# Kernel tuning notes

Hardware: AMD Instinct MI355X
Metric: run time of the kernel (lower is better)

Reference implementation:

```python
import jax, jax.numpy as jnp
import numpy as np

N, LDIMS, HID, HID2 = 1024, 256, 128, 64


def setup_inputs() -> dict:
    key = jax.random.key(0)
    ks = jax.random.split(key, 8)
    return {
        "x": jax.random.normal(ks[0], (N, 2, LDIMS), dtype=jnp.float32),
        "W_foh": jax.random.normal(ks[1], (2 * LDIMS, HID), dtype=jnp.float32) * 0.05,
        "W_fom": jax.random.normal(ks[2], (2 * LDIMS, HID), dtype=jnp.float32) * 0.05,
        "cat_bias": jax.random.normal(ks[3], (2 * HID,), dtype=jnp.float32) * 0.05,
        "W_hid2": jax.random.normal(ks[4], (2 * HID, HID2), dtype=jnp.float32) * 0.05,
        "hid2_bias": jax.random.normal(ks[5], (HID2,), dtype=jnp.float32) * 0.05,
        "W_out": jax.random.normal(ks[6], (HID2, 1), dtype=jnp.float32) * 0.05,
        "out_bias": jax.random.normal(ks[7], (1,), dtype=jnp.float32) * 0.05,
    }


def reference(x, W_foh, W_fom, cat_bias, W_hid2, hid2_bias, W_out, out_bias):
    n = x.shape[0]
    h = W_foh.shape[1]
    xf = x.reshape(n, -1)                      # concat(lstms_0, lstms_1) -> [n, 2*ldims]
    headfov = xf @ W_foh                       # [n, h]
    modfov = xf @ W_fom                        # [n, h]
    # Original: tanh(concat(headfov_i, modfov_j) + catBias) @ W_hid2.
    # tanh is elementwise, and concat @ W_hid2 splits exactly into top/bottom blocks,
    # so we precompute per-node terms instead of materializing [n, n, 2h].
    th = jnp.tanh(headfov + cat_bias[:h]) @ W_hid2[:h]    # [n, hid2]
    tm = jnp.tanh(modfov + cat_bias[h:]) @ W_hid2[h:]     # [n, hid2]
    pre = th[:, None, :] + tm[None, :, :] + hid2_bias     # [n, n, hid2]
    h2 = jnp.tanh(pre)
    scores = jnp.einsum('ijd,do->ijo', h2, W_out)[..., 0] + out_bias[0]  # [n, n]
    return scores
```

## Files before the change

### kernel.cpp

```cpp
#include <hip/hip_runtime.h>
#include <hip/hip_bf16.h>
#include <stdint.h>

typedef __attribute__((ext_vector_type(8))) short bf16x8;
typedef __attribute__((ext_vector_type(4))) float f32x4;

#define NN 1024
#define KD 512
#define NC 256
#define H2 64

#define OFF_A    0
#define OFF_WT   1048576
#define OFF_WHB  1310720
#define OFF_G    1343488
#define OFF_PT   1867776
#define OFF_QT   2129920

#define TANH_SCALE 2.8853900817779268f

static __device__ __forceinline__ ushort f2bf(float f) {
    uint32_t u = __builtin_bit_cast(uint32_t, f);
    uint32_t r = (u + 0x7fffu + ((u >> 16) & 1u)) >> 16;
    return (ushort)r;
}

__global__ __launch_bounds__(256) void k0_pack(const float* __restrict__ x,
                                               const float* __restrict__ W_foh,
                                               const float* __restrict__ W_fom,
                                               const float* __restrict__ W_hid2,
                                               ushort* __restrict__ A,
                                               ushort* __restrict__ Wt,
                                               ushort* __restrict__ Whb) {
    int tid = blockIdx.x * 256 + threadIdx.x;
    if (tid < 131072) {
        float4 v = ((const float4*)x)[tid];
        ushort4 o;
        o.x = f2bf(v.x); o.y = f2bf(v.y); o.z = f2bf(v.z); o.w = f2bf(v.w);
        ((ushort4*)A)[tid] = o;
    } else if (tid < 262144) {
        int t2 = tid - 131072;
        int c = t2 & 255, k = t2 >> 8;
        float v = (c < 128) ? W_foh[k * 128 + c] : W_fom[k * 128 + c - 128];
        Wt[c * 512 + k] = f2bf(v);
    } else if (tid < 278528) {
        int t3 = tid - 262144;
        int d = t3 & 63, c = t3 >> 6;
        Whb[d * 256 + c] = f2bf(W_hid2[c * 64 + d]);
    }
}

__global__ __launch_bounds__(256) void k1_gemm1(const ushort* __restrict__ A,
                                                const ushort* __restrict__ Wt,
                                                const float* __restrict__ cat_bias,
                                                ushort* __restrict__ g) {
    int lane = threadIdx.x & 63;
    int wave = threadIdx.x >> 6;
    int b = blockIdx.x;
    int ntile = b & 15;
    int mtile = (b >> 4) * 4 + wave;
    int l15 = lane & 15;
    int kofs = (lane >> 4) * 8;
    const ushort* Ar = A + (mtile * 16 + l15) * 512 + kofs;
    const ushort* Br = Wt + (ntile * 16 + l15) * 512 + kofs;
    f32x4 acc = {0.f, 0.f, 0.f, 0.f};
#pragma unroll
    for (int s = 0; s < 16; ++s) {
        bf16x8 a = *(const bf16x8*)(Ar + s * 32);
        bf16x8 bb = *(const bf16x8*)(Br + s * 32);
        acc = __builtin_amdgcn_mfma_f32_16x16x32_bf16(a, bb, acc, 0, 0, 0);
    }
    int col = ntile * 16 + l15;
    float cb = cat_bias[col];
#pragma unroll
    for (int r = 0; r < 4; ++r) {
        int row = mtile * 16 + (lane >> 4) * 4 + r;
        float xv = acc[r] + cb;
        float e = exp2f(xv * TANH_SCALE);
        float t = 1.0f - 2.0f * __builtin_amdgcn_rcpf(e + 1.0f);
        g[row * 256 + col] = f2bf(t);
    }
}

__global__ __launch_bounds__(256) void k2_gemm2(const ushort* __restrict__ g,
                                                const ushort* __restrict__ Whb,
                                                const float* __restrict__ hid2_bias,
                                                float* __restrict__ Pt,
                                                float* __restrict__ Qt) {
    int lane = threadIdx.x & 63;
    int wv = blockIdx.x * 4 + (threadIdx.x >> 6);
    int mtile = wv & 63;
    int dtile = (wv >> 6) & 3;
    int half = wv >> 8;
    int cbase = half * 128;
    int l15 = lane & 15;
    int kofs = (lane >> 4) * 8;
    const ushort* Ar = g + (mtile * 16 + l15) * 256 + cbase + kofs;
    const ushort* Br = Whb + (dtile * 16 + l15) * 256 + cbase + kofs;
    f32x4 acc = {0.f, 0.f, 0.f, 0.f};
#pragma unroll
    for (int s = 0; s < 4; ++s) {
        bf16x8 a = *(const bf16x8*)(Ar + s * 32);
        bf16x8 bb = *(const bf16x8*)(Br + s * 32);
        acc = __builtin_amdgcn_mfma_f32_16x16x32_bf16(a, bb, acc, 0, 0, 0);
    }
    int dcol = dtile * 16 + l15;
    float* out = half ? Qt : Pt;
    float badd = half ? 0.0f : hid2_bias[dcol];
#pragma unroll
    for (int r = 0; r < 4; ++r) {
        int i = mtile * 16 + (lane >> 4) * 4 + r;
        out[dcol * 1024 + i] = (acc[r] + badd) * TANH_SCALE;
    }
}

__global__ __launch_bounds__(256) void k3_scores(const float* __restrict__ Pt,
                                                 const float* __restrict__ Qt,
                                                 const float* __restrict__ W_out,
                                                 const float* __restrict__ out_bias,
                                                 float* __restrict__ out) {
    __shared__ float Pl[64][68];
    __shared__ float Ql[64][68];
    __shared__ float wl[64];
    int t = threadIdx.x;
    int b = blockIdx.x;
    int i0 = (b >> 4) * 64;
    int j0 = (b & 15) * 64;
    {
        int rowd = t >> 2;
        int cch = (t & 3) * 16;
        const float4* ps = (const float4*)(Pt + rowd * 1024 + i0 + cch);
        const float4* qs = (const float4*)(Qt + rowd * 1024 + j0 + cch);
#pragma unroll
        for (int u = 0; u < 4; ++u) {
            *(float4*)(&Pl[rowd][cch + u * 4]) = ps[u];
            *(float4*)(&Ql[rowd][cch + u * 4]) = qs[u];
        }
    }
    if (t < 64) wl[t] = -2.0f * W_out[t];
    float base = out_bias[0];
#pragma unroll
    for (int d = 0; d < 64; ++d) base += W_out[d];
    __syncthreads();

    int il = (t & 15) * 4;
    int jl = (t >> 4) * 4;
    float acc[4][4] = {};
#pragma unroll 4
    for (int d = 0; d < 64; ++d) {
        f32x4 p = *(const f32x4*)(&Pl[d][il]);
        f32x4 q = *(const f32x4*)(&Ql[d][jl]);
        float w = wl[d];
#pragma unroll
        for (int a = 0; a < 4; ++a)
#pragma unroll
            for (int c = 0; c < 4; ++c) {
                float e = exp2f(p[a] + q[c]);
                float r = __builtin_amdgcn_rcpf(e + 1.0f);
                acc[a][c] = fmaf(w, r, acc[a][c]);
            }
    }
#pragma unroll
    for (int a = 0; a < 4; ++a) {
        float4 v;
        v.x = base + acc[a][0];
        v.y = base + acc[a][1];
        v.z = base + acc[a][2];
        v.w = base + acc[a][3];
        *(float4*)(&out[(i0 + il + a) * 1024 + j0 + jl]) = v;
    }
}

extern "C" void kernel_launch(void* const* d_in, const int* in_sizes, int n_in,
                              void* d_out, int out_size, void* d_ws, size_t ws_size,
                              hipStream_t stream) {
    const float* x        = (const float*)d_in[0];
    const float* W_foh    = (const float*)d_in[1];
    const float* W_fom    = (const float*)d_in[2];
    const float* cat_bias = (const float*)d_in[3];
    const float* W_hid2   = (const float*)d_in[4];
    const float* hid2_bias= (const float*)d_in[5];
    const float* W_out    = (const float*)d_in[6];
    const float* out_bias = (const float*)d_in[7];

    char* ws = (char*)d_ws;
    ushort* A   = (ushort*)(ws + OFF_A);
    ushort* Wt  = (ushort*)(ws + OFF_WT);
    ushort* Whb = (ushort*)(ws + OFF_WHB);
    ushort* g   = (ushort*)(ws + OFF_G);
    float*  Pt  = (float*)(ws + OFF_PT);
    float*  Qt  = (float*)(ws + OFF_QT);

    k0_pack<<<1088, 256, 0, stream>>>(x, W_foh, W_fom, W_hid2, A, Wt, Whb);
    k1_gemm1<<<256, 256, 0, stream>>>(A, Wt, cat_bias, g);
    k2_gemm2<<<128, 256, 0, stream>>>(g, Whb, hid2_bias, Pt, Qt);
    k3_scores<<<256, 256, 0, stream>>>(Pt, Qt, W_out, out_bias, (float*)d_out);
}
```

Baseline: 104.4 us.

## Split-K gemm1 across waves and halve score tile width for more blocks

The first GEMM now splits the K dimension across the four waves of a block and reduces the partial sums through shared memory, launching four times as many blocks. The scores kernel uses 64x32 tiles instead of 64x64, doubling the block count to 512 so more CUs are occupied. The aim is to fill the 256-CU device better in both kernels. The cost is an extra shared-memory reduction and barrier in gemm1, and more redundant P loads per output in the scores kernel.

```diff
diff --git a/kernel.cpp b/kernel.cpp
--- a/kernel.cpp
+++ b/kernel.cpp
@@ -54,31 +54,40 @@
                                                 const ushort* __restrict__ Wt,
                                                 const float* __restrict__ cat_bias,
                                                 ushort* __restrict__ g) {
+    __shared__ float red[4 * 64 * 4];
     int lane = threadIdx.x & 63;
     int wave = threadIdx.x >> 6;
     int b = blockIdx.x;
     int ntile = b & 15;
-    int mtile = (b >> 4) * 4 + wave;
+    int mtile = b >> 4;
     int l15 = lane & 15;
-    int kofs = (lane >> 4) * 8;
+    int kofs = wave * 128 + (lane >> 4) * 8;
     const ushort* Ar = A + (mtile * 16 + l15) * 512 + kofs;
     const ushort* Br = Wt + (ntile * 16 + l15) * 512 + kofs;
     f32x4 acc = {0.f, 0.f, 0.f, 0.f};
 #pragma unroll
-    for (int s = 0; s < 16; ++s) {
+    for (int s = 0; s < 4; ++s) {
         bf16x8 a = *(const bf16x8*)(Ar + s * 32);
         bf16x8 bb = *(const bf16x8*)(Br + s * 32);
         acc = __builtin_amdgcn_mfma_f32_16x16x32_bf16(a, bb, acc, 0, 0, 0);
     }
-    int col = ntile * 16 + l15;
-    float cb = cat_bias[col];
-#pragma unroll
-    for (int r = 0; r < 4; ++r) {
-        int row = mtile * 16 + (lane >> 4) * 4 + r;
-        float xv = acc[r] + cb;
-        float e = exp2f(xv * TANH_SCALE);
-        float t = 1.0f - 2.0f * __builtin_amdgcn_rcpf(e + 1.0f);
-        g[row * 256 + col] = f2bf(t);
+    *(f32x4*)(&red[(wave * 64 + lane) * 4]) = acc;
+    __syncthreads();
+    if (wave == 0) {
+        f32x4 s0 = *(const f32x4*)(&red[(0 * 64 + lane) * 4]);
+        f32x4 s1 = *(const f32x4*)(&red[(1 * 64 + lane) * 4]);
+        f32x4 s2 = *(const f32x4*)(&red[(2 * 64 + lane) * 4]);
+        f32x4 s3 = *(const f32x4*)(&red[(3 * 64 + lane) * 4]);
+        int col = ntile * 16 + l15;
+        float cb = cat_bias[col];
+#pragma unroll
+        for (int r = 0; r < 4; ++r) {
+            int row = mtile * 16 + (lane >> 4) * 4 + r;
+            float xv = s0[r] + s1[r] + s2[r] + s3[r] + cb;
+            float e = exp2f(xv * TANH_SCALE);
+            float t = 1.0f - 2.0f * __builtin_amdgcn_rcpf(e + 1.0f);
+            g[row * 256 + col] = f2bf(t);
+        }
     }
 }
 
@@ -120,22 +129,25 @@
                                                  const float* __restrict__ out_bias,
                                                  float* __restrict__ out) {
     __shared__ float Pl[64][68];
-    __shared__ float Ql[64][68];
+    __shared__ float Ql[64][36];
     __shared__ float wl[64];
     int t = threadIdx.x;
     int b = blockIdx.x;
-    int i0 = (b >> 4) * 64;
-    int j0 = (b & 15) * 64;
+    int i0 = (b >> 5) * 64;
+    int j0 = (b & 31) * 32;
     {
         int rowd = t >> 2;
         int cch = (t & 3) * 16;
         const float4* ps = (const float4*)(Pt + rowd * 1024 + i0 + cch);
+#pragma unroll
+        for (int u = 0; u < 4; ++u) *(float4*)(&Pl[rowd][cch + u * 4]) = ps[u];
+    }
+    {
+        int rowd = t >> 2;
+        int cch = (t & 3) * 8;
         const float4* qs = (const float4*)(Qt + rowd * 1024 + j0 + cch);
-#pragma unroll
-        for (int u = 0; u < 4; ++u) {
-            *(float4*)(&Pl[rowd][cch + u * 4]) = ps[u];
-            *(float4*)(&Ql[rowd][cch + u * 4]) = qs[u];
-        }
+        *(float4*)(&Ql[rowd][cch]) = qs[0];
+        *(float4*)(&Ql[rowd][cch + 4]) = qs[1];
     }
     if (t < 64) wl[t] = -2.0f * W_out[t];
     float base = out_bias[0];
@@ -144,30 +156,29 @@
     __syncthreads();
 
     int il = (t & 15) * 4;
-    int jl = (t >> 4) * 4;
-    float acc[4][4] = {};
-#pragma unroll 4
+    int jl = (t >> 4) * 2;
+    float acc[4][2] = {};
+#pragma unroll 8
     for (int d = 0; d < 64; ++d) {
         f32x4 p = *(const f32x4*)(&Pl[d][il]);
-        f32x4 q = *(const f32x4*)(&Ql[d][jl]);
+        float q0 = Ql[d][jl], q1 = Ql[d][jl + 1];
         float w = wl[d];
 #pragma unroll
-        for (int a = 0; a < 4; ++a)
-#pragma unroll
-            for (int c = 0; c < 4; ++c) {
-                float e = exp2f(p[a] + q[c]);
-                float r = __builtin_amdgcn_rcpf(e + 1.0f);
-                acc[a][c] = fmaf(w, r, acc[a][c]);
-            }
+        for (int a = 0; a < 4; ++a) {
+            float e0 = exp2f(p[a] + q0);
+            float r0 = __builtin_amdgcn_rcpf(e0 + 1.0f);
+            acc[a][0] = fmaf(w, r0, acc[a][0]);
+            float e1 = exp2f(p[a] + q1);
+            float r1 = __builtin_amdgcn_rcpf(e1 + 1.0f);
+            acc[a][1] = fmaf(w, r1, acc[a][1]);
+        }
     }
 #pragma unroll
     for (int a = 0; a < 4; ++a) {
-        float4 v;
+        float2 v;
         v.x = base + acc[a][0];
         v.y = base + acc[a][1];
-        v.z = base + acc[a][2];
-        v.w = base + acc[a][3];
-        *(float4*)(&out[(i0 + il + a) * 1024 + j0 + jl]) = v;
+        *(float2*)(&out[(i0 + il + a) * 1024 + j0 + jl]) = v;
     }
 }
 
@@ -192,7 +203,7 @@
     float*  Qt  = (float*)(ws + OFF_QT);
 
     k0_pack<<<1088, 256, 0, stream>>>(x, W_foh, W_fom, W_hid2, A, Wt, Whb);
-    k1_gemm1<<<256, 256, 0, stream>>>(A, Wt, cat_bias, g);
+    k1_gemm1<<<1024, 256, 0, stream>>>(A, Wt, cat_bias, g);
     k2_gemm2<<<128, 256, 0, stream>>>(g, Whb, hid2_bias, Pt, Qt);
-    k3_scores<<<256, 256, 0, stream>>>(Pt, Qt, W_out, out_bias, (float*)d_out);
-}
+    k3_scores<<<512, 256, 0, stream>>>(Pt, Qt, W_out, out_bias, (float*)d_out);
+}
```

Result: no change. 103.9 us (-0.5%).
